# Kernel optimization log

Measured on AMD Instinct MI355X. Metric: run time of the kernel, lower is better.

The kernel has to match this reference:

```python
import jax, jax.numpy as jnp
from jax import lax
import numpy as np

B = 8192
NUM_CTX = 300; NUM_STN = 300; NUM_GPE = 20; NUM_GPI = 2; NUM_OUT = 20
FF_DIM = 20; FF_STEPS = 20; STN_ITERS = 50
ETA_GPE = 1.0; ETA_STN = 1.0 / 3.0; ETA_GPI = 0.1
A1 = 1.0; A2 = 1.0; THETAD1 = 0.0; THETAD2 = 0.0
UNITS = (64, 128, 64)

_SPECS = [("vf0", UNITS[0], NUM_CTX), ("vf1", UNITS[1], UNITS[0]), ("vf2", UNITS[2], UNITS[1]), ("vf3", 1, UNITS[2]),
          ("jd1", FF_DIM, NUM_CTX), ("jd2", FF_DIM, NUM_CTX), ("kd1", FF_DIM, NUM_CTX), ("kd2", FF_DIM, NUM_CTX),
          ("sg", NUM_GPE, NUM_STN), ("gs", NUM_STN, NUM_GPE), ("glat", NUM_GPE, NUM_GPE), ("slat", NUM_STN, NUM_STN),
          ("d1gpi", NUM_GPI, FF_DIM), ("stngpi", NUM_GPI, NUM_STN),
          ("ih", 4 * NUM_OUT, NUM_GPI), ("hh", 4 * NUM_OUT, NUM_OUT)]


def _lin_init(k, out_d, in_d):
    kw, kb = jax.random.split(k)
    bound = 1.0 / np.sqrt(in_d)
    w = jax.random.uniform(kw, (out_d, in_d), minval=-bound, maxval=bound, dtype=jnp.float32)
    b = jax.random.uniform(kb, (out_d,), minval=-bound, maxval=bound, dtype=jnp.float32)
    return w, b


def setup_inputs() -> dict:
    key = jax.random.key(0)
    ks = iter(jax.random.split(key, 40))
    inp = {}
    inp["stimulus"] = jax.random.normal(next(ks), (B, NUM_CTX), dtype=jnp.float32)
    inp["deltavf"] = jax.random.normal(next(ks), (B, 1), dtype=jnp.float32)
    inp["hx0"] = jax.random.uniform(next(ks), (B, NUM_OUT), dtype=jnp.float32)
    inp["cx0"] = jax.random.uniform(next(ks), (B, NUM_OUT), dtype=jnp.float32)
    for name, o, i in _SPECS:
        w, b = _lin_init(next(ks), o, i)
        inp["w_" + name] = w
        inp["b_" + name] = b
    return inp


def _lin(x, w, b):
    return x @ w.T + b


def _lstm_cell(x, h, c, w_ih, b_ih, w_hh, b_hh):
    gates = _lin(x, w_ih, b_ih) + _lin(h, w_hh, b_hh)
    i, f, g, o = jnp.split(gates, 4, axis=-1)  # torch LSTMCell gate order
    c_new = jax.nn.sigmoid(f) * c + jax.nn.sigmoid(i) * jnp.tanh(g)
    h_new = jax.nn.sigmoid(o) * jnp.tanh(c_new)
    return h_new, c_new


def reference(stimulus, deltavf, hx0, cx0,
              w_vf0, b_vf0, w_vf1, b_vf1, w_vf2, b_vf2, w_vf3, b_vf3,
              w_jd1, b_jd1, w_jd2, b_jd2, w_kd1, b_kd1, w_kd2, b_kd2,
              w_sg, b_sg, w_gs, b_gs, w_glat, b_glat, w_slat, b_slat,
              w_d1gpi, b_d1gpi, w_stngpi, b_stngpi,
              w_ih, b_ih, w_hh, b_hh):
    bsz = stimulus.shape[0]
    # value function head
    h = jax.nn.relu(_lin(stimulus, w_vf0, b_vf0))
    h = jax.nn.relu(_lin(h, w_vf1, b_vf1))
    h = jax.nn.relu(_lin(h, w_vf2, b_vf2))
    vt = jnp.tanh(_lin(h, w_vf3, b_vf3))  # [B, 1]

    lamd1 = jax.nn.sigmoid(A1 * (deltavf - THETAD1))  # [B, 1]
    lamd2 = jax.nn.sigmoid(A2 * (deltavf - THETAD2))  # [B, 1]

    # loop-invariant striatal drives (computed every iter in torch, same value)
    J_D1 = _lin(stimulus, w_jd1, b_jd1)
    J_D2 = _lin(stimulus, w_jd2, b_jd2)
    K_D1 = _lin(stimulus, w_kd1, b_kd1)
    K_D2 = _lin(stimulus, w_kd2, b_kd2)

    def ff_step(carry, _):
        v1, v2 = carry
        v1 = jax.nn.sigmoid(lamd1 * (J_D1 * (1.0 - v1) + (1.0 - K_D1) * v1))
        v2 = jax.nn.sigmoid(lamd2 * (J_D2 * (1.0 - v2) + (1.0 - K_D2) * v2))
        return (v1, v2), None

    z_ff = jnp.zeros((bsz, FF_DIM), dtype=stimulus.dtype)
    (V_D1, V_D2), _ = lax.scan(ff_step, (z_ff, z_ff), None, length=FF_STEPS)

    V_GPi_DP = _lin(V_D1, w_d1gpi, b_d1gpi)  # [B, num_gpi]

    def stn_step(carry, _):
        xgpe, xstn, vstn, vgpi, hx, cx = carry
        xgpe = xgpe + ETA_GPE * (-xgpe + _lin(vstn, w_sg, b_sg) + _lin(xgpe, w_glat, b_glat) - V_D2)
        xstn = xstn + ETA_STN * (-xstn + _lin(xgpe, w_gs, b_gs) + _lin(vstn, w_slat, b_slat))
        vstn = jnp.tanh(lamd2 * xstn)
        V_GPi_IP = lamd2 * _lin(vstn, w_stngpi, b_stngpi)
        vgpi = vgpi + ETA_GPI * (-vgpi - V_GPi_DP + 2.0 * V_GPi_IP)
        hx, cx = _lstm_cell(-vgpi, hx, cx, w_ih, b_ih, w_hh, b_hh)
        return (xgpe, xstn, vstn, vgpi, hx, cx), None

    carry0 = (jnp.zeros((bsz, NUM_GPE), dtype=stimulus.dtype),
              jnp.zeros((bsz, NUM_STN), dtype=stimulus.dtype),
              jnp.zeros((bsz, NUM_STN), dtype=stimulus.dtype),  # tanh(lamd2*0) = 0
              jnp.zeros((bsz, NUM_GPI), dtype=stimulus.dtype),
              hx0, cx0)
    carry, _ = lax.scan(stn_step, carry0, None, length=STN_ITERS)
    hx = carry[4]
    return hx, vt
```

## Files before the change

### kernel.cpp

```cpp
#include <hip/hip_runtime.h>


typedef _Float16 f16_t;
typedef _Float16 f16x8 __attribute__((ext_vector_type(8)));
typedef _Float16 f16x4 __attribute__((ext_vector_type(4)));
typedef float floatx4 __attribute__((ext_vector_type(4)));
typedef float floatx2 __attribute__((ext_vector_type(2)));

#define BTOT 8192
#define BM   32
#define NTHR 768
#define NBLK 256
#define VSTR 328
#define XST  32

struct Params {
  const float *stimulus, *deltavf, *hx0, *cx0;
  const float *w_vf0, *b_vf0, *w_vf1, *b_vf1, *w_vf2, *b_vf2, *w_vf3, *b_vf3;
  const float *w_jd1, *b_jd1, *w_jd2, *b_jd2, *w_kd1, *b_kd1, *w_kd2, *b_kd2;
  const float *w_sg, *b_sg, *w_gs, *b_gs, *w_glat, *b_glat, *w_slat, *b_slat;
  const float *w_d1gpi, *b_d1gpi, *w_stngpi, *b_stngpi;
  const float *w_ih, *b_ih, *w_hh, *b_hh;
  float* out;
};

struct __align__(16) Smem {
  f16_t vstn[BM * VSTR];
  f16_t xgpe[2][BM * XST];
  f16_t hxf[BM * XST];
  f16_t wB2[21 * 512];
  f16_t wsp[10 * 512];
  f16_t whh[5 * 512];
  union { float h1f[BM * 128]; float scr[3200]; float gates[BM * 80]; } u;
  float h0f[BM * 64];
  float V_D2f[BM * 20];
  float pp[3][64];
  float bsumS[304];
  float bsg[20];
  float bihh[80], wih0[80], wih1[80];
  float DPs[BM * 2], lamS[BM];
};

__device__ __forceinline__ float rcp_f(float x) { return __builtin_amdgcn_rcpf(x); }
__device__ __forceinline__ float sigm_fast(float x) { return rcp_f(1.f + __expf(-x)); }
__device__ __forceinline__ float tanh_fast(float x) { return 1.f - 2.f * rcp_f(1.f + __expf(2.f * x)); }

__device__ __forceinline__ f16x8 ldfrag(const float* row, int k0, int kmax, bool valid) {
  float4 z = make_float4(0.f, 0.f, 0.f, 0.f);
  int nv = valid ? (kmax - k0) : 0;
  float4 f0 = (nv >= 4) ? *(const float4*)(row + k0) : z;
  float4 f1 = (nv >= 8) ? *(const float4*)(row + k0 + 4) : z;
  f16x8 r;
  r[0] = (f16_t)f0.x; r[1] = (f16_t)f0.y; r[2] = (f16_t)f0.z; r[3] = (f16_t)f0.w;
  r[4] = (f16_t)f1.x; r[5] = (f16_t)f1.y; r[6] = (f16_t)f1.z; r[7] = (f16_t)f1.w;
  return r;
}

__global__ __launch_bounds__(NTHR, 3) void bg_main(Params P) {
  __shared__ Smem S;
  const int tid  = threadIdx.x;
  const int lane = tid & 63;
  const int wv   = tid >> 6;
  const int q    = lane >> 4;
  const int cl   = lane & 15;
  const int row0 = blockIdx.x * BM;
  const floatx4 zf = {0.f, 0.f, 0.f, 0.f};

  const int  t0s  = wv;
  const int  t1s  = (wv < 7) ? (12 + wv) : (wv == 7 ? 19 : (wv == 8 ? 20 : 255));
  const bool has1 = (t1s != 255);
  const bool isSg = (t1s == 19 || t1s == 20);
  const bool gs1  = (t1s < 19);
  const int  gtile = (wv >= 9) ? (wv - 9) : (wv == 7 ? 3 : (wv == 8 ? 4 : -1));

  if (tid < BM) S.lamS[tid] = sigm_fast(P.deltavf[row0 + tid]);
  for (int i = tid; i < 2 * BM * XST; i += NTHR) ((f16_t*)S.xgpe)[i] = (f16_t)0.f;
  for (int i = tid; i < BM * XST; i += NTHR) {
    int m = i >> 5, j = i & 31;
    S.hxf[i] = (j < 20) ? (f16_t)P.hx0[row0 * 20 + m * 20 + j] : (f16_t)0.f;
  }
  for (int i = tid; i < BM * VSTR; i += NTHR) S.vstn[i] = (f16_t)0.f;
  for (int i = tid; i < 21 * 512; i += NTHR) {
    int t = i >> 9, l = (i >> 3) & 63, jj = i & 7;
    int c2 = l & 15, k = ((l >> 4) << 3) + jj;
    float v = 0.f;
    if (t < 19) { int n = t * 16 + c2; if (n < 300 && k < 20) v = P.w_gs[n * 20 + k]; }
    else        { int g = (t - 19) * 16 + c2; if (g < 20 && k < 20) v = P.w_glat[g * 20 + k]; }
    S.wB2[i] = (f16_t)v;
  }
  for (int i = tid; i < 10 * 512; i += NTHR) {
    int c = i >> 9, l = (i >> 3) & 63, jj = i & 7;
    int p = l & 15, k = c * 32 + ((l >> 4) << 3) + jj;
    float v = (p < 2 && k < 300) ? P.w_stngpi[p * 300 + k] : 0.f;
    S.wsp[i] = (f16_t)v;
  }
  for (int i = tid; i < 5 * 512; i += NTHR) {
    int t = i >> 9, l = (i >> 3) & 63, jj = i & 7;
    int g = t * 16 + (l & 15), k = ((l >> 4) << 3) + jj;
    S.whh[i] = (f16_t)((k < 20) ? P.w_hh[g * 20 + k] : 0.f);
  }
  for (int i = tid; i < 304; i += NTHR) S.bsumS[i] = (i < 300) ? (P.b_slat[i] + P.b_gs[i]) : 0.f;
  for (int i = tid; i < 20; i += NTHR)  S.bsg[i] = P.b_sg[i] + P.b_glat[i];
  for (int i = tid; i < 80; i += NTHR) {
    S.bihh[i] = P.b_ih[i] + P.b_hh[i];
    S.wih0[i] = P.w_ih[i * 2 + 0];
    S.wih1[i] = P.w_ih[i * 2 + 1];
  }

  if (tid < 512) {
    int o = tid & 63, mb = (tid >> 6) * 4;
    const float4* wr = (const float4*)(P.w_vf0 + o * 300);
    float bias = P.b_vf0[o], a[4];
#pragma unroll
    for (int u = 0; u < 4; ++u) a[u] = bias;
    for (int kq = 0; kq < 75; ++kq) {
      float4 w = wr[kq];
#pragma unroll
      for (int u = 0; u < 4; ++u) {
        float4 v = *(const float4*)(P.stimulus + (size_t)(row0 + mb + u) * 300 + kq * 4);
        a[u] = fmaf(v.x, w.x, a[u]); a[u] = fmaf(v.y, w.y, a[u]);
        a[u] = fmaf(v.z, w.z, a[u]); a[u] = fmaf(v.w, w.w, a[u]);
      }
    }
#pragma unroll
    for (int u = 0; u < 4; ++u) S.h0f[(mb + u) * 64 + o] = fmaxf(a[u], 0.f);
  }
  __syncthreads();
  if (tid < 512) {
    int o = tid & 127, mb = (tid >> 7) * 8;
    const float* wr = P.w_vf1 + o * 64;
    float bias = P.b_vf1[o], a[8];
#pragma unroll
    for (int u = 0; u < 8; ++u) a[u] = bias;
    for (int k = 0; k < 64; ++k) {
      float w = wr[k];
#pragma unroll
      for (int u = 0; u < 8; ++u) a[u] = fmaf(S.h0f[(mb + u) * 64 + k], w, a[u]);
    }
#pragma unroll
    for (int u = 0; u < 8; ++u) S.u.h1f[(mb + u) * 128 + o] = fmaxf(a[u], 0.f);
  }
  __syncthreads();
  if (tid < 512) {
    int o = tid & 63, mb = (tid >> 6) * 4;
    const float* wr = P.w_vf2 + o * 128;
    float bias = P.b_vf2[o], a[4];
#pragma unroll
    for (int u = 0; u < 4; ++u) a[u] = bias;
    for (int k = 0; k < 128; ++k) {
      float w = wr[k];
#pragma unroll
      for (int u = 0; u < 4; ++u) a[u] = fmaf(S.u.h1f[(mb + u) * 128 + k], w, a[u]);
    }
#pragma unroll
    for (int u = 0; u < 4; ++u) S.h0f[(mb + u) * 64 + o] = fmaxf(a[u], 0.f);
  }
  __syncthreads();
  {
    int oid = tid & 127, mb = (tid >> 7) * 8;
    if (tid < 512 && oid < 80) {
      int which = oid / 20, o = oid - which * 20;
      const float *wp, *bp;
      if (which == 0)      { wp = P.w_jd1; bp = P.b_jd1; }
      else if (which == 1) { wp = P.w_jd2; bp = P.b_jd2; }
      else if (which == 2) { wp = P.w_kd1; bp = P.b_kd1; }
      else                 { wp = P.w_kd2; bp = P.b_kd2; }
      float bias = bp[o], a[8];
#pragma unroll
      for (int u = 0; u < 8; ++u) a[u] = bias;
      for (int kq = 0; kq < 75; ++kq) {
        float4 w = *(const float4*)(wp + o * 300 + kq * 4);
#pragma unroll
        for (int u = 0; u < 8; ++u) {
          float4 v = *(const float4*)(P.stimulus + (size_t)(row0 + mb + u) * 300 + kq * 4);
          a[u] = fmaf(v.x, w.x, a[u]); a[u] = fmaf(v.y, w.y, a[u]);
          a[u] = fmaf(v.z, w.z, a[u]); a[u] = fmaf(v.w, w.w, a[u]);
        }
      }
#pragma unroll
      for (int u = 0; u < 8; ++u) S.u.scr[which * 640 + (mb + u) * 20 + o] = a[u];
    }
    if (tid < BM) {
      float a = P.b_vf3[0];
      for (int k = 0; k < 64; ++k) a = fmaf(S.h0f[tid * 64 + k], P.w_vf3[k], a);
      P.out[(size_t)BTOT * 20 + row0 + tid] = tanh_fast(a);
    }
  }
  __syncthreads();
  for (int i = tid; i < BM * 20; i += NTHR) {
    int m = i / 20;
    float j1 = S.u.scr[i],        j2 = S.u.scr[640 + i];
    float k1 = S.u.scr[1280 + i], k2 = S.u.scr[1920 + i];
    float L = S.lamS[m], v1 = 0.f, v2 = 0.f;
    for (int s = 0; s < 20; ++s) {
      v1 = sigm_fast(L * (j1 * (1.f - v1) + (1.f - k1) * v1));
      v2 = sigm_fast(L * (j2 * (1.f - v2) + (1.f - k2) * v2));
    }
    S.u.scr[2560 + i] = v1;
    S.V_D2f[i] = v2;
  }
  __syncthreads();
  if (tid < BM * 2) {
    int m = tid >> 1, p2 = tid & 1;
    float a = P.b_d1gpi[p2];
    for (int o = 0; o < 20; ++o) a = fmaf(S.u.scr[2560 + m * 20 + o], P.w_d1gpi[p2 * 20 + o], a);
    S.DPs[tid] = a;
  }
  __syncthreads();

  const float lam0 = S.lamS[cl], lam1 = S.lamS[cl + 16];
  const float bstn0 = P.b_stngpi[0], bstn1 = P.b_stngpi[1];
  const bool lown = (tid < BM * 20);
  const int  m0 = lown ? tid / 20 : 0;
  const int  j0 = tid - m0 * 20;
  const float lamr = S.lamS[m0];
  const float DP0 = S.DPs[m0 * 2], DP1 = S.DPs[m0 * 2 + 1];
  float cxr0 = lown ? P.cx0[row0 * 20 + tid] : 0.f;
  float hxr0 = 0.f;
  float vg0 = 0.f, vg1 = 0.f;

  f16x8 Ws[2][10];
  {
    int n = t0s * 16 + cl;
    const float* a0 = P.w_slat + (size_t)n * 300;
#pragma unroll
    for (int c = 0; c < 10; ++c) Ws[0][c] = ldfrag(a0, c * 32 + q * 8, 300, true);
    if (t1s < 19) {
      int n1 = t1s * 16 + cl;
      const float* a1 = P.w_slat + (size_t)(n1 < 300 ? n1 : 0) * 300;
#pragma unroll
      for (int c = 0; c < 10; ++c) Ws[1][c] = ldfrag(a1, c * 32 + q * 8, 300, n1 < 300);
    } else if (isSg) {
      int g = (t1s - 19) * 16 + cl;
      const float* a1 = P.w_sg + (size_t)(g < 20 ? g : 0) * 300;
#pragma unroll
      for (int c = 0; c < 10; ++c) Ws[1][c] = ldfrag(a1, c * 32 + q * 8, 300, g < 20);
    } else {
      f16x8 z;
#pragma unroll
      for (int e = 0; e < 8; ++e) z[e] = (f16_t)0.f;
#pragma unroll
      for (int c = 0; c < 10; ++c) Ws[1][c] = z;
    }
  }

  float xs[2][2][4];
#pragma unroll
  for (int j = 0; j < 2; ++j)
#pragma unroll
    for (int mf = 0; mf < 2; ++mf)
#pragma unroll
      for (int r = 0; r < 4; ++r) xs[j][mf][r] = 0.f;

  for (int it = 0; it < 50; ++it) {
    const int po = it & 1, pn = po ^ 1;
    floatx4 acc[2][2];
    acc[0][0] = zf; acc[0][1] = zf; acc[1][0] = zf; acc[1][1] = zf;

    __builtin_amdgcn_s_setprio(1);
    if (has1) {
#pragma unroll
      for (int c = 0; c < 10; ++c) {
        f16x8 b0 = *(const f16x8*)&S.vstn[cl * VSTR + c * 32 + q * 8];
        f16x8 b1 = *(const f16x8*)&S.vstn[(16 + cl) * VSTR + c * 32 + q * 8];
        acc[0][0] = __builtin_amdgcn_mfma_f32_16x16x32_f16(Ws[0][c], b0, acc[0][0], 0, 0, 0);
        acc[0][1] = __builtin_amdgcn_mfma_f32_16x16x32_f16(Ws[0][c], b1, acc[0][1], 0, 0, 0);
        acc[1][0] = __builtin_amdgcn_mfma_f32_16x16x32_f16(Ws[1][c], b0, acc[1][0], 0, 0, 0);
        acc[1][1] = __builtin_amdgcn_mfma_f32_16x16x32_f16(Ws[1][c], b1, acc[1][1], 0, 0, 0);
      }
    } else {
#pragma unroll
      for (int c = 0; c < 10; ++c) {
        f16x8 b0 = *(const f16x8*)&S.vstn[cl * VSTR + c * 32 + q * 8];
        f16x8 b1 = *(const f16x8*)&S.vstn[(16 + cl) * VSTR + c * 32 + q * 8];
        acc[0][0] = __builtin_amdgcn_mfma_f32_16x16x32_f16(Ws[0][c], b0, acc[0][0], 0, 0, 0);
        acc[0][1] = __builtin_amdgcn_mfma_f32_16x16x32_f16(Ws[0][c], b1, acc[0][1], 0, 0, 0);
      }
    }
    __builtin_amdgcn_s_setprio(0);
    if (isSg) {
      f16x8 Wg = *(const f16x8*)&S.wB2[t1s * 512 + lane * 8];
      f16x8 g0 = *(const f16x8*)&S.xgpe[po][cl * XST + q * 8];
      f16x8 g1 = *(const f16x8*)&S.xgpe[po][(16 + cl) * XST + q * 8];
      acc[1][0] = __builtin_amdgcn_mfma_f32_16x16x32_f16(Wg, g0, acc[1][0], 0, 0, 0);
      acc[1][1] = __builtin_amdgcn_mfma_f32_16x16x32_f16(Wg, g1, acc[1][1], 0, 0, 0);
      int g0i = (t1s - 19) * 16 + q * 4;
      if (g0i < 20) {
        floatx4 bg4 = *(const floatx4*)&S.bsg[g0i];
#pragma unroll
        for (int mf = 0; mf < 2; ++mf) {
          int batch = cl + 16 * mf;
          floatx4 vd4 = *(const floatx4*)&S.V_D2f[batch * 20 + g0i];
          f16x4 pk;
#pragma unroll
          for (int r = 0; r < 4; ++r) pk[r] = (f16_t)(acc[1][mf][r] + bg4[r] - vd4[r]);
          *(f16x4*)&S.xgpe[pn][batch * XST + g0i] = pk;
        }
      }
    }
    __syncthreads();

    {
      f16x8 x0 = *(const f16x8*)&S.xgpe[pn][cl * XST + q * 8];
      f16x8 x1 = *(const f16x8*)&S.xgpe[pn][(16 + cl) * XST + q * 8];
      {
        f16x8 Wg0 = *(const f16x8*)&S.wB2[t0s * 512 + lane * 8];
        acc[0][0] = __builtin_amdgcn_mfma_f32_16x16x32_f16(Wg0, x0, acc[0][0], 0, 0, 0);
        acc[0][1] = __builtin_amdgcn_mfma_f32_16x16x32_f16(Wg0, x1, acc[0][1], 0, 0, 0);
      }
      if (gs1) {
        f16x8 Wg1 = *(const f16x8*)&S.wB2[t1s * 512 + lane * 8];
        acc[1][0] = __builtin_amdgcn_mfma_f32_16x16x32_f16(Wg1, x0, acc[1][0], 0, 0, 0);
        acc[1][1] = __builtin_amdgcn_mfma_f32_16x16x32_f16(Wg1, x1, acc[1][1], 0, 0, 0);
      }
      if (gtile >= 0) {
        f16x8 Wh = *(const f16x8*)&S.whh[gtile * 512 + lane * 8];
        f16x8 h0 = *(const f16x8*)&S.hxf[cl * XST + q * 8];
        f16x8 h1 = *(const f16x8*)&S.hxf[(16 + cl) * XST + q * 8];
        floatx4 gA = __builtin_amdgcn_mfma_f32_16x16x32_f16(Wh, h0, zf, 0, 0, 0);
        floatx4 gB = __builtin_amdgcn_mfma_f32_16x16x32_f16(Wh, h1, zf, 0, 0, 0);
        int gb = gtile * 16 + q * 4;
        *(floatx4*)&S.u.gates[cl * 80 + gb] = gA;
        *(floatx4*)&S.u.gates[(cl + 16) * 80 + gb] = gB;
      }
#pragma unroll
      for (int j = 0; j < 2; ++j) {
        int t = j ? t1s : t0s;
        if (t < 19) {
          int n0 = t * 16 + q * 4;
          if (!(t == 18 && q == 3)) {
            floatx4 bs4 = *(const floatx4*)&S.bsumS[n0];
#pragma unroll
            for (int mf = 0; mf < 2; ++mf) {
              float lm = mf ? lam1 : lam0;
              f16x4 pk;
#pragma unroll
              for (int r = 0; r < 4; ++r) {
                float xo = xs[j][mf][r];
                float xn = xo + (1.0f / 3.0f) * (acc[j][mf][r] + bs4[r] - xo);
                xs[j][mf][r] = xn;
                pk[r] = (f16_t)tanh_fast(lm * xn);
              }
              *(f16x4*)&S.vstn[(cl + 16 * mf) * VSTR + n0] = pk;
            }
          }
        }
      }
    }
    __syncthreads();

    if (wv >= 9) {
      const int c0 = (wv == 9) ? 0 : (wv == 10 ? 4 : 7);
      const int c1 = (wv == 9) ? 4 : (wv == 10 ? 7 : 10);
      floatx4 ip0 = zf, ip1 = zf;
      for (int c = c0; c < c1; ++c) {
        f16x8 Wp = *(const f16x8*)&S.wsp[c * 512 + lane * 8];
        f16x8 b0 = *(const f16x8*)&S.vstn[cl * VSTR + c * 32 + q * 8];
        f16x8 b1 = *(const f16x8*)&S.vstn[(16 + cl) * VSTR + c * 32 + q * 8];
        ip0 = __builtin_amdgcn_mfma_f32_16x16x32_f16(Wp, b0, ip0, 0, 0, 0);
        ip1 = __builtin_amdgcn_mfma_f32_16x16x32_f16(Wp, b1, ip1, 0, 0, 0);
      }
      if (q == 0) {
        floatx2 w0; w0[0] = ip0[0]; w0[1] = ip0[1];
        floatx2 w1; w1[0] = ip1[0]; w1[1] = ip1[1];
        *(floatx2*)&S.pp[wv - 9][cl * 2] = w0;
        *(floatx2*)&S.pp[wv - 9][(16 + cl) * 2] = w1;
      }
    }
    __syncthreads();

    if (lown) {
      float s0 = S.pp[0][m0 * 2]     + S.pp[1][m0 * 2]     + S.pp[2][m0 * 2];
      float s1 = S.pp[0][m0 * 2 + 1] + S.pp[1][m0 * 2 + 1] + S.pp[2][m0 * 2 + 1];
      float ipa = lamr * (s0 + bstn0);
      float ipb = lamr * (s1 + bstn1);
      vg0 = vg0 + 0.1f * (-vg0 - DP0 + 2.f * ipa);
      vg1 = vg1 + 0.1f * (-vg1 - DP1 + 2.f * ipb);
      float gi = S.u.gates[m0 * 80 + j0]      + S.bihh[j0]      - S.wih0[j0] * vg0      - S.wih1[j0] * vg1;
      float gf = S.u.gates[m0 * 80 + 20 + j0] + S.bihh[20 + j0] - S.wih0[20 + j0] * vg0 - S.wih1[20 + j0] * vg1;
      float gg = S.u.gates[m0 * 80 + 40 + j0] + S.bihh[40 + j0] - S.wih0[40 + j0] * vg0 - S.wih1[40 + j0] * vg1;
      float go = S.u.gates[m0 * 80 + 60 + j0] + S.bihh[60 + j0] - S.wih0[60 + j0] * vg0 - S.wih1[60 + j0] * vg1;
      float cn = sigm_fast(gf) * cxr0 + sigm_fast(gi) * tanh_fast(gg);
      cxr0 = cn;
      hxr0 = sigm_fast(go) * tanh_fast(cn);
      S.hxf[m0 * XST + j0] = (f16_t)hxr0;
    }
  }

  if (lown) P.out[(size_t)row0 * 20 + tid] = hxr0;
}

extern "C" void kernel_launch(void* const* d_in, const int* in_sizes, int n_in,
                              void* d_out, int out_size, void* d_ws, size_t ws_size,
                              hipStream_t stream) {
  (void)in_sizes; (void)n_in; (void)out_size; (void)d_ws; (void)ws_size;
  Params P;
  P.stimulus = (const float*)d_in[0];
  P.deltavf  = (const float*)d_in[1];
  P.hx0 = (const float*)d_in[2];
  P.cx0 = (const float*)d_in[3];
  P.w_vf0 = (const float*)d_in[4];  P.b_vf0 = (const float*)d_in[5];
  P.w_vf1 = (const float*)d_in[6];  P.b_vf1 = (const float*)d_in[7];
  P.w_vf2 = (const float*)d_in[8];  P.b_vf2 = (const float*)d_in[9];
  P.w_vf3 = (const float*)d_in[10]; P.b_vf3 = (const float*)d_in[11];
  P.w_jd1 = (const float*)d_in[12]; P.b_jd1 = (const float*)d_in[13];
  P.w_jd2 = (const float*)d_in[14]; P.b_jd2 = (const float*)d_in[15];
  P.w_kd1 = (const float*)d_in[16]; P.b_kd1 = (const float*)d_in[17];
  P.w_kd2 = (const float*)d_in[18]; P.b_kd2 = (const float*)d_in[19];
  P.w_sg  = (const float*)d_in[20]; P.b_sg  = (const float*)d_in[21];
  P.w_gs  = (const float*)d_in[22]; P.b_gs  = (const float*)d_in[23];
  P.w_glat= (const float*)d_in[24]; P.b_glat= (const float*)d_in[25];
  P.w_slat= (const float*)d_in[26]; P.b_slat= (const float*)d_in[27];
  P.w_d1gpi  = (const float*)d_in[28]; P.b_d1gpi  = (const float*)d_in[29];
  P.w_stngpi = (const float*)d_in[30]; P.b_stngpi = (const float*)d_in[31];
  P.w_ih = (const float*)d_in[32]; P.b_ih = (const float*)d_in[33];
  P.w_hh = (const float*)d_in[34]; P.b_hh = (const float*)d_in[35];
  P.out  = (float*)d_out;
  bg_main<<<NBLK, NTHR, 0, stream>>>(P);
}
```

Before: 406.1 us.

## Fuse STN-to-GPi projection into tanh epilogue and drop a barrier

Removes the separate MFMA pass over vstn that computed the STN-to-GPi projection on dedicated waves. Each wave now accumulates the two-output dot product in fp32 during its tanh epilogue, reduces it across quads with lane shuffles, and writes per-wave partials that the LSTM threads sum, which eliminates one __syncthreads per iteration. Tile assignment is rebalanced: the GPe tiles move to waves 7 and 8, waves 9 and 10 take STN tiles 7 and 8, and the LSTM threads shift to tid>=128. LSTM biases and input weights are hoisted into registers. The costs are extra register pressure, shuffle work, and a 12-way partial sum per LSTM thread.

```diff
diff --git a/kernel.cpp b/kernel.cpp
--- a/kernel.cpp
+++ b/kernel.cpp
@@ -13,6 +13,7 @@
 #define NBLK 256
 #define VSTR 328
 #define XST  32
+#define LBASE 128
 
 struct Params {
   const float *stimulus, *deltavf, *hx0, *cx0;
@@ -29,12 +30,12 @@
   f16_t xgpe[2][BM * XST];
   f16_t hxf[BM * XST];
   f16_t wB2[21 * 512];
-  f16_t wsp[10 * 512];
   f16_t whh[5 * 512];
   union { float h1f[BM * 128]; float scr[3200]; float gates[BM * 80]; } u;
   float h0f[BM * 64];
   float V_D2f[BM * 20];
-  float pp[3][64];
+  float pp[12][64];
+  float wspf[2][304];
   float bsumS[304];
   float bsg[20];
   float bihh[80], wih0[80], wih1[80];
@@ -56,7 +57,23 @@
   return r;
 }
 
-__global__ __launch_bounds__(NTHR, 3) void bg_main(Params P) {
+__device__ __forceinline__ void load_tile(const Params& P, int t, int cl, int q, f16x8* dst) {
+  if (t < 19) {
+    int n = t * 16 + cl;
+    const float* a = P.w_slat + (size_t)(n < 300 ? n : 0) * 300;
+#pragma unroll
+    for (int c = 0; c < 10; ++c) dst[c] = ldfrag(a, c * 32 + q * 8, 300, n < 300);
+  } else {
+    int g = (t - 19) * 16 + cl;
+    const float* a = P.w_sg + (size_t)(g < 20 ? g : 0) * 300;
+#pragma unroll
+    for (int c = 0; c < 10; ++c) dst[c] = ldfrag(a, c * 32 + q * 8, 300, g < 20);
+  }
+}
+
+__global__ __launch_bounds__(NTHR)
+__attribute__((amdgpu_waves_per_eu(3, 3)))
+void bg_main(Params P) {
   __shared__ Smem S;
   const int tid  = threadIdx.x;
   const int lane = tid & 63;
@@ -66,12 +83,15 @@
   const int row0 = blockIdx.x * BM;
   const floatx4 zf = {0.f, 0.f, 0.f, 0.f};
 
-  const int  t0s  = wv;
-  const int  t1s  = (wv < 7) ? (12 + wv) : (wv == 7 ? 19 : (wv == 8 ? 20 : 255));
-  const bool has1 = (t1s != 255);
-  const bool isSg = (t1s == 19 || t1s == 20);
-  const bool gs1  = (t1s < 19);
-  const int  gtile = (wv >= 9) ? (wv - 9) : (wv == 7 ? 3 : (wv == 8 ? 4 : -1));
+  int s0 = wv, s1 = -1;
+  if (wv < 7)        { s1 = 12 + wv; }
+  else if (wv == 7)  { s0 = 19; }
+  else if (wv == 8)  { s0 = 20; }
+  else if (wv == 9)  { s1 = 7; }
+  else if (wv == 10) { s1 = 8; }
+  const bool isSg = (s0 >= 19);
+  const bool has1 = (s1 >= 0);
+  const int  gtile = (wv >= 7) ? (wv == 7 ? 3 : (wv == 8 ? 4 : wv - 9)) : -1;
 
   if (tid < BM) S.lamS[tid] = sigm_fast(P.deltavf[row0 + tid]);
   for (int i = tid; i < 2 * BM * XST; i += NTHR) ((f16_t*)S.xgpe)[i] = (f16_t)0.f;
@@ -88,16 +108,14 @@
     else        { int g = (t - 19) * 16 + c2; if (g < 20 && k < 20) v = P.w_glat[g * 20 + k]; }
     S.wB2[i] = (f16_t)v;
   }
-  for (int i = tid; i < 10 * 512; i += NTHR) {
-    int c = i >> 9, l = (i >> 3) & 63, jj = i & 7;
-    int p = l & 15, k = c * 32 + ((l >> 4) << 3) + jj;
-    float v = (p < 2 && k < 300) ? P.w_stngpi[p * 300 + k] : 0.f;
-    S.wsp[i] = (f16_t)v;
-  }
   for (int i = tid; i < 5 * 512; i += NTHR) {
     int t = i >> 9, l = (i >> 3) & 63, jj = i & 7;
     int g = t * 16 + (l & 15), k = ((l >> 4) << 3) + jj;
     S.whh[i] = (f16_t)((k < 20) ? P.w_hh[g * 20 + k] : 0.f);
+  }
+  for (int i = tid; i < 2 * 304; i += NTHR) {
+    int p = i / 304, k = i - p * 304;
+    S.wspf[p][k] = (k < 300) ? P.w_stngpi[p * 300 + k] : 0.f;
   }
   for (int i = tid; i < 304; i += NTHR) S.bsumS[i] = (i < 300) ? (P.b_slat[i] + P.b_gs[i]) : 0.f;
   for (int i = tid; i < 20; i += NTHR)  S.bsg[i] = P.b_sg[i] + P.b_glat[i];
@@ -210,38 +228,31 @@
 
   const float lam0 = S.lamS[cl], lam1 = S.lamS[cl + 16];
   const float bstn0 = P.b_stngpi[0], bstn1 = P.b_stngpi[1];
-  const bool lown = (tid < BM * 20);
-  const int  m0 = lown ? tid / 20 : 0;
-  const int  j0 = tid - m0 * 20;
+  const bool lown = (tid >= LBASE);
+  const int  eL = lown ? (tid - LBASE) : 0;
+  const int  m0 = eL / 20, j0 = eL - m0 * 20;
   const float lamr = S.lamS[m0];
   const float DP0 = S.DPs[m0 * 2], DP1 = S.DPs[m0 * 2 + 1];
-  float cxr0 = lown ? P.cx0[row0 * 20 + tid] : 0.f;
+  const float bi_i = S.bihh[j0],      bi_f = S.bihh[20 + j0];
+  const float bi_g = S.bihh[40 + j0], bi_o = S.bihh[60 + j0];
+  const float wA_i = S.wih0[j0],      wA_f = S.wih0[20 + j0];
+  const float wA_g = S.wih0[40 + j0], wA_o = S.wih0[60 + j0];
+  const float wB_i = S.wih1[j0],      wB_f = S.wih1[20 + j0];
+  const float wB_g = S.wih1[40 + j0], wB_o = S.wih1[60 + j0];
+  float cxr0 = lown ? P.cx0[row0 * 20 + eL] : 0.f;
   float hxr0 = 0.f;
   float vg0 = 0.f, vg1 = 0.f;
 
   f16x8 Ws[2][10];
-  {
-    int n = t0s * 16 + cl;
-    const float* a0 = P.w_slat + (size_t)n * 300;
-#pragma unroll
-    for (int c = 0; c < 10; ++c) Ws[0][c] = ldfrag(a0, c * 32 + q * 8, 300, true);
-    if (t1s < 19) {
-      int n1 = t1s * 16 + cl;
-      const float* a1 = P.w_slat + (size_t)(n1 < 300 ? n1 : 0) * 300;
-#pragma unroll
-      for (int c = 0; c < 10; ++c) Ws[1][c] = ldfrag(a1, c * 32 + q * 8, 300, n1 < 300);
-    } else if (isSg) {
-      int g = (t1s - 19) * 16 + cl;
-      const float* a1 = P.w_sg + (size_t)(g < 20 ? g : 0) * 300;
-#pragma unroll
-      for (int c = 0; c < 10; ++c) Ws[1][c] = ldfrag(a1, c * 32 + q * 8, 300, g < 20);
-    } else {
-      f16x8 z;
-#pragma unroll
-      for (int e = 0; e < 8; ++e) z[e] = (f16_t)0.f;
-#pragma unroll
-      for (int c = 0; c < 10; ++c) Ws[1][c] = z;
-    }
+  load_tile(P, s0, cl, q, Ws[0]);
+  if (has1) {
+    load_tile(P, s1, cl, q, Ws[1]);
+  } else {
+    f16x8 z;
+#pragma unroll
+    for (int e = 0; e < 8; ++e) z[e] = (f16_t)0.f;
+#pragma unroll
+    for (int c = 0; c < 10; ++c) Ws[1][c] = z;
   }
 
   float xs[2][2][4];
@@ -279,12 +290,12 @@
     }
     __builtin_amdgcn_s_setprio(0);
     if (isSg) {
-      f16x8 Wg = *(const f16x8*)&S.wB2[t1s * 512 + lane * 8];
+      f16x8 Wg = *(const f16x8*)&S.wB2[s0 * 512 + lane * 8];
       f16x8 g0 = *(const f16x8*)&S.xgpe[po][cl * XST + q * 8];
       f16x8 g1 = *(const f16x8*)&S.xgpe[po][(16 + cl) * XST + q * 8];
-      acc[1][0] = __builtin_amdgcn_mfma_f32_16x16x32_f16(Wg, g0, acc[1][0], 0, 0, 0);
-      acc[1][1] = __builtin_amdgcn_mfma_f32_16x16x32_f16(Wg, g1, acc[1][1], 0, 0, 0);
-      int g0i = (t1s - 19) * 16 + q * 4;
+      acc[0][0] = __builtin_amdgcn_mfma_f32_16x16x32_f16(Wg, g0, acc[0][0], 0, 0, 0);
+      acc[0][1] = __builtin_amdgcn_mfma_f32_16x16x32_f16(Wg, g1, acc[0][1], 0, 0, 0);
+      int g0i = (s0 - 19) * 16 + q * 4;
       if (g0i < 20) {
         floatx4 bg4 = *(const floatx4*)&S.bsg[g0i];
 #pragma unroll
@@ -293,23 +304,24 @@
           floatx4 vd4 = *(const floatx4*)&S.V_D2f[batch * 20 + g0i];
           f16x4 pk;
 #pragma unroll
-          for (int r = 0; r < 4; ++r) pk[r] = (f16_t)(acc[1][mf][r] + bg4[r] - vd4[r]);
+          for (int r = 0; r < 4; ++r) pk[r] = (f16_t)(acc[0][mf][r] + bg4[r] - vd4[r]);
           *(f16x4*)&S.xgpe[pn][batch * XST + g0i] = pk;
         }
       }
     }
     __syncthreads();
 
+    float sp00 = 0.f, sp01 = 0.f, sp10 = 0.f, sp11 = 0.f;
     {
       f16x8 x0 = *(const f16x8*)&S.xgpe[pn][cl * XST + q * 8];
       f16x8 x1 = *(const f16x8*)&S.xgpe[pn][(16 + cl) * XST + q * 8];
-      {
-        f16x8 Wg0 = *(const f16x8*)&S.wB2[t0s * 512 + lane * 8];
+      if (s0 < 19) {
+        f16x8 Wg0 = *(const f16x8*)&S.wB2[s0 * 512 + lane * 8];
         acc[0][0] = __builtin_amdgcn_mfma_f32_16x16x32_f16(Wg0, x0, acc[0][0], 0, 0, 0);
         acc[0][1] = __builtin_amdgcn_mfma_f32_16x16x32_f16(Wg0, x1, acc[0][1], 0, 0, 0);
       }
-      if (gs1) {
-        f16x8 Wg1 = *(const f16x8*)&S.wB2[t1s * 512 + lane * 8];
+      if (has1) {
+        f16x8 Wg1 = *(const f16x8*)&S.wB2[s1 * 512 + lane * 8];
         acc[1][0] = __builtin_amdgcn_mfma_f32_16x16x32_f16(Wg1, x0, acc[1][0], 0, 0, 0);
         acc[1][1] = __builtin_amdgcn_mfma_f32_16x16x32_f16(Wg1, x1, acc[1][1], 0, 0, 0);
       }
@@ -325,11 +337,13 @@
       }
 #pragma unroll
       for (int j = 0; j < 2; ++j) {
-        int t = j ? t1s : t0s;
-        if (t < 19) {
+        int t = j ? s1 : s0;
+        if (t >= 0 && t < 19) {
           int n0 = t * 16 + q * 4;
           if (!(t == 18 && q == 3)) {
             floatx4 bs4 = *(const floatx4*)&S.bsumS[n0];
+            floatx4 w0 = *(const floatx4*)&S.wspf[0][n0];
+            floatx4 w1 = *(const floatx4*)&S.wspf[1][n0];
 #pragma unroll
             for (int mf = 0; mf < 2; ++mf) {
               float lm = mf ? lam1 : lam0;
@@ -339,47 +353,44 @@
                 float xo = xs[j][mf][r];
                 float xn = xo + (1.0f / 3.0f) * (acc[j][mf][r] + bs4[r] - xo);
                 xs[j][mf][r] = xn;
-                pk[r] = (f16_t)tanh_fast(lm * xn);
+                float vv = tanh_fast(lm * xn);
+                pk[r] = (f16_t)vv;
+                if (mf) { sp01 = fmaf(w0[r], vv, sp01); sp11 = fmaf(w1[r], vv, sp11); }
+                else    { sp00 = fmaf(w0[r], vv, sp00); sp10 = fmaf(w1[r], vv, sp10); }
               }
               *(f16x4*)&S.vstn[(cl + 16 * mf) * VSTR + n0] = pk;
             }
           }
         }
       }
+      sp00 += __shfl_xor(sp00, 16); sp00 += __shfl_xor(sp00, 32);
+      sp01 += __shfl_xor(sp01, 16); sp01 += __shfl_xor(sp01, 32);
+      sp10 += __shfl_xor(sp10, 16); sp10 += __shfl_xor(sp10, 32);
+      sp11 += __shfl_xor(sp11, 16); sp11 += __shfl_xor(sp11, 32);
+      if (q == 0) {
+        floatx2 a; a[0] = sp00; a[1] = sp10;
+        floatx2 b; b[0] = sp01; b[1] = sp11;
+        *(floatx2*)&S.pp[wv][cl * 2] = a;
+        *(floatx2*)&S.pp[wv][32 + cl * 2] = b;
+      }
     }
     __syncthreads();
 
-    if (wv >= 9) {
-      const int c0 = (wv == 9) ? 0 : (wv == 10 ? 4 : 7);
-      const int c1 = (wv == 9) ? 4 : (wv == 10 ? 7 : 10);
-      floatx4 ip0 = zf, ip1 = zf;
-      for (int c = c0; c < c1; ++c) {
-        f16x8 Wp = *(const f16x8*)&S.wsp[c * 512 + lane * 8];
-        f16x8 b0 = *(const f16x8*)&S.vstn[cl * VSTR + c * 32 + q * 8];
-        f16x8 b1 = *(const f16x8*)&S.vstn[(16 + cl) * VSTR + c * 32 + q * 8];
-        ip0 = __builtin_amdgcn_mfma_f32_16x16x32_f16(Wp, b0, ip0, 0, 0, 0);
-        ip1 = __builtin_amdgcn_mfma_f32_16x16x32_f16(Wp, b1, ip1, 0, 0, 0);
-      }
-      if (q == 0) {
-        floatx2 w0; w0[0] = ip0[0]; w0[1] = ip0[1];
-        floatx2 w1; w1[0] = ip1[0]; w1[1] = ip1[1];
-        *(floatx2*)&S.pp[wv - 9][cl * 2] = w0;
-        *(floatx2*)&S.pp[wv - 9][(16 + cl) * 2] = w1;
-      }
-    }
-    __syncthreads();
-
     if (lown) {
-      float s0 = S.pp[0][m0 * 2]     + S.pp[1][m0 * 2]     + S.pp[2][m0 * 2];
-      float s1 = S.pp[0][m0 * 2 + 1] + S.pp[1][m0 * 2 + 1] + S.pp[2][m0 * 2 + 1];
-      float ipa = lamr * (s0 + bstn0);
-      float ipb = lamr * (s1 + bstn1);
+      float sA = 0.f, sB = 0.f;
+#pragma unroll
+      for (int w = 0; w < 12; ++w) {
+        floatx2 t2 = *(const floatx2*)&S.pp[w][m0 * 2];
+        sA += t2[0]; sB += t2[1];
+      }
+      float ipa = lamr * (sA + bstn0);
+      float ipb = lamr * (sB + bstn1);
       vg0 = vg0 + 0.1f * (-vg0 - DP0 + 2.f * ipa);
       vg1 = vg1 + 0.1f * (-vg1 - DP1 + 2.f * ipb);
-      float gi = S.u.gates[m0 * 80 + j0]      + S.bihh[j0]      - S.wih0[j0] * vg0      - S.wih1[j0] * vg1;
-      float gf = S.u.gates[m0 * 80 + 20 + j0] + S.bihh[20 + j0] - S.wih0[20 + j0] * vg0 - S.wih1[20 + j0] * vg1;
-      float gg = S.u.gates[m0 * 80 + 40 + j0] + S.bihh[40 + j0] - S.wih0[40 + j0] * vg0 - S.wih1[40 + j0] * vg1;
-      float go = S.u.gates[m0 * 80 + 60 + j0] + S.bihh[60 + j0] - S.wih0[60 + j0] * vg0 - S.wih1[60 + j0] * vg1;
+      float gi = S.u.gates[m0 * 80 + j0]      + bi_i - wA_i * vg0 - wB_i * vg1;
+      float gf = S.u.gates[m0 * 80 + 20 + j0] + bi_f - wA_f * vg0 - wB_f * vg1;
+      float gg = S.u.gates[m0 * 80 + 40 + j0] + bi_g - wA_g * vg0 - wB_g * vg1;
+      float go = S.u.gates[m0 * 80 + 60 + j0] + bi_o - wA_o * vg0 - wB_o * vg1;
       float cn = sigm_fast(gf) * cxr0 + sigm_fast(gi) * tanh_fast(gg);
       cxr0 = cn;
       hxr0 = sigm_fast(go) * tanh_fast(cn);
@@ -387,7 +398,7 @@
     }
   }
 
-  if (lown) P.out[(size_t)row0 * 20 + tid] = hxr0;
+  if (lown) P.out[(size_t)row0 * 20 + eL] = hxr0;
 }
 
 extern "C" void kernel_launch(void* const* d_in, const int* in_sizes, int n_in,
```

New measurement: 452.6 us. 11.5% more time.
